# Optimization experiments

Measured on AMD Instinct MI355X. Metric: run time of the kernel, lower is better.

The kernel has to match this reference:

```python
import jax, jax.numpy as jnp
import numpy as np


def _rotated_kernels(kernel, n_or):
    """Nearest-neighbour rotated copies of the kernel.

    kernel: [C, kOr, kH, kW] -> returns [n_or, C, kOr, kH, kW] where slice t is the
    kernel sampled at R_{2*pi*t/n_or}(y', x') about the kernel center; rotated
    coordinates that fall outside the kernel grid contribute zero.
    """
    C, kOr, kH, kW = kernel.shape
    cy = (kH - 1) / 2.0
    cx = (kW - 1) / 2.0
    ang = 2.0 * jnp.pi * jnp.arange(n_or, dtype=jnp.float32) / n_or
    ca = jnp.cos(ang)[:, None, None]  # [n_or,1,1]
    sa = jnp.sin(ang)[:, None, None]
    yy = jnp.arange(kH, dtype=jnp.float32)[:, None] - cy  # [kH,1]
    xx = jnp.arange(kW, dtype=jnp.float32)[None, :] - cx  # [1,kW]
    # rotate grid points by angle theta
    ys = sa * xx + ca * yy  # [n_or,kH,kW]
    xs = ca * xx - sa * yy
    iy = jnp.round(ys + cy).astype(jnp.int32)
    ix = jnp.round(xs + cx).astype(jnp.int32)
    mask = ((iy >= 0) & (iy < kH) & (ix >= 0) & (ix < kW)).astype(kernel.dtype)
    iyc = jnp.clip(iy, 0, kH - 1)
    ixc = jnp.clip(ix, 0, kW - 1)
    rot = kernel[:, :, iyc, ixc]            # [C,kOr,n_or,kH,kW] (gather)
    rot = rot * mask[None, None]            # zero out-of-grid samples
    return jnp.transpose(rot, (2, 0, 1, 3, 4))  # [n_or,C,kOr,kH,kW]


def setup_inputs() -> dict:
    key = jax.random.key(0)
    k1, k2 = jax.random.split(key)
    B, C, Or, H, W = 8, 32, 8, 128, 128
    kOr, kH, kW = 8, 5, 5
    x = jax.random.normal(k1, (B, C, Or, H, W), dtype=jnp.float32)
    # module parameter: uniform(-1, 1) per reset_parameters()
    kernel = jax.random.uniform(k2, (C, kOr, kH, kW), minval=-1.0, maxval=1.0,
                                dtype=jnp.float32)
    return {"x": x, "kernel": kernel}


def reference(x, kernel):
    """SE(2) linear (depthwise) group convolution.

    out[b,c,t,y,x] = sum_{t',y',x'} x[b,c,(t+t')%Or, y+y', x+x']
                     * kernel[c, t', NN(R_{2pi t/Or}(y', x'))]
    with centered, zero-padded spatial offsets ('SAME').
    """
    B, C, Or, H, W = x.shape
    _, kOr, kH, kW = kernel.shape
    rotk = _rotated_kernels(kernel, Or)  # [Or,C,kOr,kH,kW]
    dn = ('NCHW', 'OIHW', 'NCHW')
    out = jnp.zeros((B, C * Or, H, W), dtype=x.dtype)
    for tp in range(kOr):  # small fixed orientation-offset loop
        xs = jnp.roll(x, -tp, axis=2).reshape(B, C * Or, H, W)  # circular wrap in Or
        k = jnp.transpose(rotk[:, :, tp], (1, 0, 2, 3)).reshape(C * Or, 1, kH, kW)
        out = out + jax.lax.conv_general_dilated(
            xs, k, window_strides=(1, 1), padding='SAME',
            feature_group_count=C * Or, dimension_numbers=dn)
    return out.reshape(B, C, Or, H, W)
```

## Files before the change

### kernel.cpp

```cpp
#include <hip/hip_runtime.h>


typedef short bf16x8 __attribute__((ext_vector_type(8)));
typedef float f32x4 __attribute__((ext_vector_type(4)));

__device__ inline unsigned short f2bf(float f) {
    unsigned int u = __float_as_uint(f);
    u += 0x7fffu + ((u >> 16) & 1u);
    return (unsigned short)(u >> 16);
}
__device__ inline unsigned pk2(float a, float b) {
    return (unsigned)f2bf(a) | ((unsigned)f2bf(b) << 16);
}

__device__ __constant__ float CA8[8] = {1.0f, 0.70710678f, 0.0f, -0.70710678f,
                                        -1.0f, -0.70710678f, 0.0f, 0.70710678f};
__device__ __constant__ float SA8[8] = {0.0f, 0.70710678f, 1.0f, 0.70710678f,
                                        0.0f, -0.70710678f, -1.0f, -0.70710678f};

__device__ inline float rot_w(const float* __restrict__ kern, int c, int t,
                              int o, int dy, int dx) {
    float ca = CA8[t], sa = SA8[t];
    float xx = (float)dx - 2.0f, yy = (float)dy - 2.0f;
    int iy = (int)rintf(sa * xx + ca * yy + 2.0f);
    int ix = (int)rintf(ca * xx - sa * yy + 2.0f);
    if (iy >= 0 && iy < 5 && ix >= 0 && ix < 5) {
        int tp = (o - t) & 7;
        return kern[(c * 8 + tp) * 25 + iy * 5 + ix];
    }
    return 0.0f;
}

__global__ __launch_bounds__(256)
void build_w2(const float* __restrict__ kern, unsigned short* __restrict__ wtab) {
    int e = blockIdx.x * 256 + threadIdx.x;
    if (e >= 131072) return;
    int o   = e & 7;
    int tr  = (e >> 3) & 31;
    int n16 = (e >> 8) & 15;
    int c   = e >> 12;
    int t   = n16 & 7, dlt = n16 >> 3;
    float w = 0.0f;
    if (tr < 30) {
        int dyr = tr / 5, dx = tr - 5 * dyr;
        int dy  = dyr - dlt;
        if (dy >= 0 && dy < 5) w = rot_w(kern, c, t, o, dy, dx);
    }
    wtab[e] = f2bf(w);
}

template <bool TAB>
__global__ __launch_bounds__(256)
void se2_mfma(const float* __restrict__ x, const float* __restrict__ kern,
              const unsigned short* __restrict__ wtab, float* __restrict__ out) {
    __shared__ __align__(16) unsigned short ldsx[36 * 36 * 8];

    const int bid = (blockIdx.x & 7) * 512 + (blockIdx.x >> 3);
    const int tx = bid & 3, ty = (bid >> 2) & 3;
    const int bc = bid >> 4;
    const int c  = bc & 31;
    const int X0 = tx * 32, Y0 = ty * 32;
    const int tid = threadIdx.x;

    const int lane = tid & 63;
    const int wv   = tid >> 6;
    const int g    = lane >> 4;
    const int m16  = lane & 15;

    const float* xbase = x + (size_t)bc * 131072;

    auto loadch = [&](int e, float (&v)[8]) {
        int r = e / 36, col = e - r * 36;
        int gy = Y0 - 2 + r, gx = X0 - 2 + col;
        if (gy >= 0 && gy < 128 && gx >= 0 && gx < 128) {
            const float* src = xbase + gy * 128 + gx;
#pragma unroll
            for (int o = 0; o < 8; ++o) v[o] = src[o * 16384];
        } else {
#pragma unroll
            for (int o = 0; o < 8; ++o) v[o] = 0.0f;
        }
    };
    auto packch = [&](int e, const float (&v)[8]) {
        *reinterpret_cast<uint4*>(&ldsx[e * 8]) =
            make_uint4(pk2(v[0], v[1]), pk2(v[2], v[3]),
                       pk2(v[4], v[5]), pk2(v[6], v[7]));
    };

    float sA[8], sB[8];
    loadch(tid, sA);
    loadch(tid + 256, sB);

    bf16x8 wfrag[8];
    int    tapoff[8];
#pragma unroll
    for (int cc = 0; cc < 8; ++cc) {
        int tr  = cc * 4 + g;
        int trc = tr < 30 ? tr : 29;
        int dyr = trc / 5, dx = trc - 5 * dyr;
        tapoff[cc] = (dyr * 36 + dx) * 8;
        if constexpr (TAB)
            wfrag[cc] = *reinterpret_cast<const bf16x8*>(
                &wtab[((c * 16 + m16) * 32 + tr) * 8]);
    }

    if constexpr (!TAB) {
        __shared__ __align__(16) unsigned short ldsw[16 * 32 * 8];
        for (int e = tid; e < 4096; e += 256) {
            int o = e & 7, tr = (e >> 3) & 31, n16 = e >> 8;
            int t = n16 & 7, dlt = n16 >> 3;
            float w = 0.0f;
            if (tr < 30) {
                int dyr = tr / 5, dx = tr - 5 * dyr;
                int dy  = dyr - dlt;
                if (dy >= 0 && dy < 5) w = rot_w(kern, c, t, o, dy, dx);
            }
            ldsw[e] = f2bf(w);
        }
        __syncthreads();
#pragma unroll
        for (int cc = 0; cc < 8; ++cc)
            wfrag[cc] = *reinterpret_cast<const bf16x8*>(
                &ldsw[(m16 * 32 + cc * 4 + g) * 8]);
    }

    packch(tid, sA);
    packch(tid + 256, sB);
    loadch(tid + 512, sA);
    loadch(tid + 768, sB);
    packch(tid + 512, sA);
    packch(tid + 768, sB);
    loadch(tid + 1024, sA);
    if (tid < 16) loadch(tid + 1280, sB);
    packch(tid + 1024, sA);
    if (tid < 16) packch(tid + 1280, sB);
    __syncthreads();

    const int t_o = m16 & 7, dlt = m16 >> 3;
    float* outl = out + (size_t)bc * 131072 + (size_t)t_o * 16384 +
                  (size_t)(Y0 + dlt) * 128 + X0 + g * 4;

#pragma unroll 2
    for (int s = 0; s < 8; ++s) {
        int pr = s >> 1;
        int xh = s & 1;
        int yl = wv * 8 + pr * 2;
        int baseS = (yl * 36 + xh * 16 + m16) * 8;
        f32x4 acc = {0.f, 0.f, 0.f, 0.f};
#pragma unroll
        for (int cc = 0; cc < 8; ++cc) {
            bf16x8 xf = *reinterpret_cast<const bf16x8*>(&ldsx[baseS + tapoff[cc]]);
            acc = __builtin_amdgcn_mfma_f32_16x16x32_bf16(xf, wfrag[cc], acc, 0, 0, 0);
        }
        *reinterpret_cast<float4*>(outl + (size_t)yl * 128 + xh * 16) =
            make_float4(acc[0], acc[1], acc[2], acc[3]);
    }
}

extern "C" void kernel_launch(void* const* d_in, const int* in_sizes, int n_in,
                              void* d_out, int out_size, void* d_ws, size_t ws_size,
                              hipStream_t stream) {
    const float* x    = (const float*)d_in[0];
    const float* kern = (const float*)d_in[1];
    float* out = (float*)d_out;
    dim3 block(256);
    if (ws_size >= 131072 * sizeof(unsigned short)) {
        unsigned short* wtab = (unsigned short*)d_ws;
        build_w2<<<dim3(512), block, 0, stream>>>(kern, wtab);
        se2_mfma<true><<<dim3(4096), block, 0, stream>>>(x, kern, wtab, out);
    } else {
        se2_mfma<false><<<dim3(4096), block, 0, stream>>>(x, kern, nullptr, out);
    }
}
```

Baseline: 62.39 us.

## Retile to 16x64 output blocks and stage outputs through LDS for coalesced stores

Changes the per-block tile from 32x32 to 16 rows by 64 columns, so each input halo row is wider and global loads and stores cover longer contiguous runs. All eight MFMA accumulators are now computed before any store, written into a padded LDS epilogue buffer, and re-read so each wave writes full 256-byte row segments per orientation. The aim is more coalesced output writes in place of the scattered 16-byte stores. In exchange it adds extra syncthreads, an LDS round trip and more live accumulator registers. The halo overhead also changes, with proportionally more halo rows.

```diff
diff --git a/kernel.cpp b/kernel.cpp
--- a/kernel.cpp
+++ b/kernel.cpp
@@ -3,6 +3,9 @@
 
 typedef short bf16x8 __attribute__((ext_vector_type(8)));
 typedef float f32x4 __attribute__((ext_vector_type(4)));
+
+#define EPIL_TS 1092
+#define EPIL_RP 68
 
 __device__ inline unsigned short f2bf(float f) {
     unsigned int u = __float_as_uint(f);
@@ -53,13 +56,16 @@
 __global__ __launch_bounds__(256)
 void se2_mfma(const float* __restrict__ x, const float* __restrict__ kern,
               const unsigned short* __restrict__ wtab, float* __restrict__ out) {
-    __shared__ __align__(16) unsigned short ldsx[36 * 36 * 8];
+    __shared__ __align__(16) float ldsbuf[8 * EPIL_TS];
+    unsigned short* stage = reinterpret_cast<unsigned short*>(ldsbuf);
+    float* epil = ldsbuf;
 
     const int bid = (blockIdx.x & 7) * 512 + (blockIdx.x >> 3);
-    const int tx = bid & 3, ty = (bid >> 2) & 3;
-    const int bc = bid >> 4;
-    const int c  = bc & 31;
-    const int X0 = tx * 32, Y0 = ty * 32;
+    const int xh2 = bid & 1;
+    const int ys  = (bid >> 1) & 7;
+    const int bc  = bid >> 4;
+    const int c   = bc & 31;
+    const int X0  = xh2 * 64, Y0 = ys * 16;
     const int tid = threadIdx.x;
 
     const int lane = tid & 63;
@@ -70,7 +76,7 @@
     const float* xbase = x + (size_t)bc * 131072;
 
     auto loadch = [&](int e, float (&v)[8]) {
-        int r = e / 36, col = e - r * 36;
+        int r = e / 68, col = e - r * 68;
         int gy = Y0 - 2 + r, gx = X0 - 2 + col;
         if (gy >= 0 && gy < 128 && gx >= 0 && gx < 128) {
             const float* src = xbase + gy * 128 + gx;
@@ -82,7 +88,7 @@
         }
     };
     auto packch = [&](int e, const float (&v)[8]) {
-        *reinterpret_cast<uint4*>(&ldsx[e * 8]) =
+        *reinterpret_cast<uint4*>(&stage[e * 8]) =
             make_uint4(pk2(v[0], v[1]), pk2(v[2], v[3]),
                        pk2(v[4], v[5]), pk2(v[6], v[7]));
     };
@@ -98,14 +104,14 @@
         int tr  = cc * 4 + g;
         int trc = tr < 30 ? tr : 29;
         int dyr = trc / 5, dx = trc - 5 * dyr;
-        tapoff[cc] = (dyr * 36 + dx) * 8;
+        tapoff[cc] = (dyr * 68 + dx) * 8;
         if constexpr (TAB)
             wfrag[cc] = *reinterpret_cast<const bf16x8*>(
                 &wtab[((c * 16 + m16) * 32 + tr) * 8]);
     }
 
     if constexpr (!TAB) {
-        __shared__ __align__(16) unsigned short ldsw[16 * 32 * 8];
+        unsigned short* ldsw = stage + 12288;
         for (int e = tid; e < 4096; e += 256) {
             int o = e & 7, tr = (e >> 3) & 31, n16 = e >> 8;
             int t = n16 & 7, dlt = n16 >> 3;
@@ -131,29 +137,46 @@
     packch(tid + 512, sA);
     packch(tid + 768, sB);
     loadch(tid + 1024, sA);
-    if (tid < 16) loadch(tid + 1280, sB);
+    if (tid < 80) loadch(tid + 1280, sB);
     packch(tid + 1024, sA);
-    if (tid < 16) packch(tid + 1280, sB);
+    if (tid < 80) packch(tid + 1280, sB);
+    __syncthreads();
+
+    f32x4 acc[8];
+#pragma unroll
+    for (int s = 0; s < 8; ++s) {
+        acc[s] = (f32x4){0.f, 0.f, 0.f, 0.f};
+        const int yl = wv * 4 + (s >> 2) * 2;
+        const int baseS = (yl * 68 + (s & 3) * 16 + m16) * 8;
+#pragma unroll
+        for (int cc = 0; cc < 8; ++cc) {
+            bf16x8 xf = *reinterpret_cast<const bf16x8*>(&stage[baseS + tapoff[cc]]);
+            acc[s] = __builtin_amdgcn_mfma_f32_16x16x32_bf16(xf, wfrag[cc], acc[s], 0, 0, 0);
+        }
+    }
     __syncthreads();
 
     const int t_o = m16 & 7, dlt = m16 >> 3;
-    float* outl = out + (size_t)bc * 131072 + (size_t)t_o * 16384 +
-                  (size_t)(Y0 + dlt) * 128 + X0 + g * 4;
+#pragma unroll
+    for (int s = 0; s < 8; ++s) {
+        int y = wv * 4 + (s >> 2) * 2 + dlt;
+        int xx = (s & 3) * 16 + g * 4;
+        *reinterpret_cast<f32x4*>(&epil[t_o * EPIL_TS + y * EPIL_RP + xx]) = acc[s];
+    }
+    __syncthreads();
 
-#pragma unroll 2
-    for (int s = 0; s < 8; ++s) {
-        int pr = s >> 1;
-        int xh = s & 1;
-        int yl = wv * 8 + pr * 2;
-        int baseS = (yl * 36 + xh * 16 + m16) * 8;
-        f32x4 acc = {0.f, 0.f, 0.f, 0.f};
+    const int xq   = lane & 15;
+    const int yloc = lane >> 4;
+    float* outb = out + (size_t)bc * 131072;
 #pragma unroll
-        for (int cc = 0; cc < 8; ++cc) {
-            bf16x8 xf = *reinterpret_cast<const bf16x8*>(&ldsx[baseS + tapoff[cc]]);
-            acc = __builtin_amdgcn_mfma_f32_16x16x32_bf16(xf, wfrag[cc], acc, 0, 0, 0);
-        }
-        *reinterpret_cast<float4*>(outl + (size_t)yl * 128 + xh * 16) =
-            make_float4(acc[0], acc[1], acc[2], acc[3]);
+    for (int j = 0; j < 8; ++j) {
+        int t = wv * 2 + (j & 1);
+        int y = (j >> 1) * 4 + yloc;
+        f32x4 v = *reinterpret_cast<const f32x4*>(
+            &epil[t * EPIL_TS + y * EPIL_RP + xq * 4]);
+        *reinterpret_cast<f32x4*>(
+            outb + (size_t)t * 16384 + (size_t)(Y0 + y) * 128 + X0 + xq * 4) =
+            v;
     }
 }
 
```

New measurement: 56.24 us. -9.9%, faster.
